# Kernel optimization log

Measured on AMD Instinct MI355X. Metric: run time of the kernel, lower is better.

## Reference

```python
import jax, jax.numpy as jnp
import numpy as np

DIM = 512
NUM_GROUPS = 32
EPS = 1e-6
INV_SQRT2 = 0.7071067811865476


def group_norm(x, gamma, beta):
    # x: [b, c, h, w]; GroupNorm with NUM_GROUPS groups, per-channel affine
    b, c, h, w = x.shape
    xg = x.reshape(b, NUM_GROUPS, c // NUM_GROUPS, h, w)
    mu = xg.mean(axis=(2, 3, 4), keepdims=True)
    var = xg.var(axis=(2, 3, 4), keepdims=True)
    xn = ((xg - mu) * jax.lax.rsqrt(var + EPS)).reshape(b, c, h, w)
    return xn * gamma[None, :, None, None] + beta[None, :, None, None]


def conv1x1(x, w, b):
    # 1x1 conv == per-pixel GEMM over channels. w: [out_c, in_c], b: [out_c]
    return jnp.einsum('oc,bchw->bohw', w, x) + b[None, :, None, None]


def setup_inputs() -> dict:
    key = jax.random.key(0)
    ks = jax.random.split(key, 6)
    b, c, h, w = 4, DIM, 64, 64
    q = jax.random.normal(ks[0], (b, c, h, w), dtype=jnp.float32)
    init = lambda k: jax.random.normal(k, (DIM, DIM), dtype=jnp.float32) * 0.02
    return {
        'q': q,
        'gamma': jnp.ones((DIM,), jnp.float32),
        'beta': jnp.zeros((DIM,), jnp.float32),
        'wq': init(ks[1]), 'bq': jnp.zeros((DIM,), jnp.float32),
        'wk': init(ks[2]), 'bk': jnp.zeros((DIM,), jnp.float32),
        'wv': init(ks[3]), 'bv': jnp.zeros((DIM,), jnp.float32),
        'wo': init(ks[4]), 'bo': jnp.zeros((DIM,), jnp.float32),
    }


def reference(q, gamma, beta, wq, bq, wk, bk, wv, bv, wo, bo):
    q_in = q
    x = group_norm(q, gamma, beta)  # self-attention path: v is None -> v = normed q
    qp = conv1x1(x, wq, bq)
    kp = conv1x1(x, wk, bk)
    vp = conv1x1(x, wv, bv)
    b, c, h, w = qp.shape
    qf = qp.reshape(b, c, h * w)
    kf = kp.reshape(b, c, h * w)
    vf = vp.reshape(b, c, h * w)
    # scores[b, i, j] = sum_c k[b,c,i] * q[b,c,j]; softmax over i (key axis, dim=-2)
    scores = jnp.einsum('bci,bcj->bij', kf, qf) * (c ** -0.5)
    attn = jax.nn.softmax(scores, axis=-2)
    out = jnp.einsum('bci,bij->bcj', vf, attn).reshape(b, c, h, w)
    out = conv1x1(out, wo, bo)
    return (out + q_in) * INV_SQRT2
```

## Files before the change

kernel.cpp:

```cpp
#include <hip/hip_runtime.h>

typedef __bf16 bf16;
typedef __bf16 bf16x4 __attribute__((ext_vector_type(4)));
typedef __bf16 bf16x8 __attribute__((ext_vector_type(8)));
typedef float floatx4 __attribute__((ext_vector_type(4)));
typedef float floatx16 __attribute__((ext_vector_type(16)));

#define SCALE_QK 0.044194173824159216f
#define INV_SQRT2F 0.7071067811865476f
#define TEN  8388608L
#define SBAT 2097152L

typedef const __attribute__((address_space(1))) void GV;
typedef __attribute__((address_space(3))) void SV;

__global__ __launch_bounds__(256) void detect_k(
    const unsigned* __restrict__ q, int* __restrict__ flag)
{
    __shared__ int cnt;
    if (threadIdx.x == 0) cnt = 0;
    __syncthreads();
    int c = 0;
    for (int i = threadIdx.x; i < 4096; i += 256) {
        unsigned e = (q[i] >> 7) & 0xFFu;
        c += (e >= 100u && e <= 140u) ? 1 : 0;
    }
    atomicAdd(&cnt, c);
    __syncthreads();
    if (threadIdx.x == 0) *flag = (cnt < 3000) ? 1 : 0;
}

__global__ __launch_bounds__(256) void convw_k(
    const void* w0, const void* w1, const void* w2, const void* w3,
    bf16* __restrict__ dst, const int* __restrict__ flag)
{
    const void* srcs[4] = {w0, w1, w2, w3};
    const void* s = srcs[blockIdx.y];
    bf16* d = dst + (size_t)blockIdx.y * 262144;
    const int i = (blockIdx.x * 256 + threadIdx.x) * 8;
    bf16x8 v;
    if (*flag) {
        const float* f = (const float*)s;
        #pragma unroll
        for (int r = 0; r < 8; ++r) v[r] = (bf16)f[i + r];
    } else {
        v = *(const bf16x8*)((const bf16*)s + i);
    }
    *(bf16x8*)(d + i) = v;
}

__global__ __launch_bounds__(256) void convp_k(
    const void* p0, const void* p1, const void* p2,
    const void* p3, const void* p4, const void* p5,
    float* __restrict__ dst, const int* __restrict__ flag)
{
    const void* srcs[6] = {p0, p1, p2, p3, p4, p5};
    const int f = *flag;
    for (int i = threadIdx.x; i < 3072; i += 256) {
        const void* s = srcs[i >> 9];
        const int off = i & 511;
        dst[i] = f ? ((const float*)s)[off] : (float)((const bf16*)s)[off];
    }
}

__global__ __launch_bounds__(256) void groupnorm_k(
    const void* __restrict__ qraw, const float* __restrict__ gamma,
    const float* __restrict__ beta, bf16* __restrict__ XN,
    const int* __restrict__ flag)
{
    const int tid = threadIdx.x;
    const int b = blockIdx.x >> 5, g = blockIdx.x & 31;
    const int f32 = *flag;
    const size_t base = ((size_t)b * 512 + (size_t)g * 16) * 4096;
    const float* sf = (const float*)qraw + base;
    const bf16*  sb = (const bf16*)qraw + base;

    float sum = 0.f, sq = 0.f;
    if (f32) {
        const floatx4* v4 = (const floatx4*)sf;
        for (int idx = tid; idx < 16384; idx += 256) {
            floatx4 v = v4[idx];
            #pragma unroll
            for (int r = 0; r < 4; ++r) { float f = v[r]; sum += f; sq += f * f; }
        }
    } else {
        const bf16x8* v8 = (const bf16x8*)sb;
        for (int idx = tid; idx < 8192; idx += 256) {
            bf16x8 v = v8[idx];
            #pragma unroll
            for (int r = 0; r < 8; ++r) { float f = (float)v[r]; sum += f; sq += f * f; }
        }
    }
    #pragma unroll
    for (int off = 32; off; off >>= 1) {
        sum += __shfl_down(sum, off);
        sq  += __shfl_down(sq, off);
    }
    __shared__ float sS[4], sQ[4];
    __shared__ float s_mean, s_rstd;
    const int wave = tid >> 6, lane = tid & 63;
    if (lane == 0) { sS[wave] = sum; sQ[wave] = sq; }
    __syncthreads();
    if (tid == 0) {
        float ts = sS[0] + sS[1] + sS[2] + sS[3];
        float tq = sQ[0] + sQ[1] + sQ[2] + sQ[3];
        float mean = ts * (1.0f / 65536.0f);
        float var  = tq * (1.0f / 65536.0f) - mean * mean;
        s_mean = mean;
        s_rstd = rsqrtf(fmaxf(var, 0.f) + 1e-6f);
    }
    __syncthreads();
    const float mean = s_mean, rstd = s_rstd;

    float ga[16], be[16];
    #pragma unroll
    for (int c = 0; c < 16; ++c) {
        ga[c] = gamma[g * 16 + c] * rstd;
        be[c] = beta[g * 16 + c] - mean * ga[c];
    }
    bf16* dst = XN + (size_t)b * SBAT + (size_t)g * 16;
    for (int p0 = 0; p0 < 4096; p0 += 256) {
        const int p = p0 + tid;
        bf16x8 o0, o1;
        #pragma unroll
        for (int c = 0; c < 8; ++c) {
            float v = f32 ? sf[(size_t)c * 4096 + p] : (float)sb[(size_t)c * 4096 + p];
            o0[c] = (bf16)(v * ga[c] + be[c]);
        }
        #pragma unroll
        for (int c = 0; c < 8; ++c) {
            float v = f32 ? sf[(size_t)(c + 8) * 4096 + p] : (float)sb[(size_t)(c + 8) * 4096 + p];
            o1[c] = (bf16)(v * ga[c + 8] + be[c + 8]);
        }
        bf16* dp = dst + (size_t)p * 512;
        *(bf16x8*)dp = o0;
        *(bf16x8*)(dp + 8) = o1;
    }
}

__global__ __launch_bounds__(512, 1) void fused_attn(
    const bf16* __restrict__ QKt,
    const bf16* __restrict__ V,
    bf16* __restrict__ AOt)
{
    __shared__ __align__(16) char smc[163840];

    const int tid = threadIdx.x;
    const int w = tid >> 6, lane = tid & 63;
    const int fr = lane & 15, quad = lane >> 4;
    const int l5 = lane >> 5, l31 = lane & 31;

    const int ll = blockIdx.x;
    const int xcd = ll & 7, rr = ll >> 3;
    const int b = xcd >> 1;
    const int j0 = ((xcd & 1) * 32 + rr) * 64;

    const bf16* Qb = QKt + (size_t)b * 4194304;
    const bf16* Kb = Qb + 512;
    const bf16* Vb = V + (size_t)b * SBAT;

    const int lcK = ((tid & 15) ^ ((tid >> 4) & 15)) << 3;
    const int rowK = tid >> 4;
    auto stageK = [&](int key0, int kd0, int buf) {
        char* d = smc + buf * 32768;
        const bf16* s0 = Kb + (size_t)(key0 + rowK) * 1024 + kd0 + lcK;
        #pragma unroll
        for (int rho = 0; rho < 4; ++rho)
            __builtin_amdgcn_global_load_lds((GV*)(s0 + (size_t)rho * 32 * 1024),
                (SV*)(d + rho * 8192 + tid * 16), 16, 0, 0);
    };
    const int lcV = ((tid & 3) ^ ((tid >> 3) & 3)) << 3;
    const int rowV = tid >> 2;
    auto stageV = [&](int i0, int buf) {
        char* d = smc + 65536 + buf * 32768;
        const bf16* s0 = Vb + (size_t)rowV * 4096 + i0 + lcV;
        #pragma unroll
        for (int rho = 0; rho < 4; ++rho)
            __builtin_amdgcn_global_load_lds((GV*)(s0 + (size_t)rho * 128 * 4096),
                (SV*)(d + rho * 8192 + tid * 16), 16, 0, 0);
    };
    auto stage_sub = [&](int cc, int s) {
        if (s < 3) {
            if (cc < 32) stageK(cc * 128, (s + 1) * 128, (s + 1) & 1);
            if (cc >= 1 && cc <= 32)
                stageV((cc - 1) * 128 + (s + 1) * 32, (s + 1) & 1);
        } else {
            if (cc < 31) stageK((cc + 1) * 128, 0, 0);
            if (cc < 32) stageV(cc * 128, 0);
        }
    };

    stageK(0, 0, 0);

    if (w < 4) {
        const int jb = w >> 1;
        const int kw = w & 1;
        bf16x8 qf[2][16];
        #pragma unroll
        for (int jj = 0; jj < 2; ++jj) {
            const bf16* qsrc = Qb +
                (size_t)(j0 + jb * 32 + jj * 16 + fr) * 1024 + quad * 8;
            #pragma unroll
            for (int s = 0; s < 16; ++s)
                qf[jj][s] = *(const bf16x8*)(qsrc + s * 32);
        }
        const int kbase = (kw * 64 + fr) * 256;
        const int pxor = fr << 4;
        const int prow0 = (jb * 32 + fr) * 256;
        const int pcol0 = kw * 128;
        float l_acc0 = 0.f, l_acc1 = 0.f;

        for (int cc = 0; cc <= 32; ++cc) {
            floatx4 acc_s[4][2] = {};
            #pragma unroll
            for (int s = 0; s < 4; ++s) {
                asm volatile("s_waitcnt vmcnt(0)" ::: "memory");
                __builtin_amdgcn_s_barrier();
                stage_sub(cc, s);
                if (cc < 32) {
                    const char* kbuf = smc + (s & 1) * 32768;
                    __builtin_amdgcn_s_setprio(1);
                    #pragma unroll
                    for (int ksl = 0; ksl < 4; ++ksl) {
                        bf16x8 kfr[4];
                        #pragma unroll
                        for (int kf = 0; kf < 4; ++kf)
                            kfr[kf] = *(const bf16x8*)(kbuf + kbase + kf * 4096 +
                                ((((ksl << 2) | quad) ^ fr) << 4));
                        #pragma unroll
                        for (int kf = 0; kf < 4; ++kf) {
                            acc_s[kf][0] = __builtin_amdgcn_mfma_f32_16x16x32_bf16(
                                kfr[kf], qf[0][s * 4 + ksl], acc_s[kf][0], 0, 0, 0);
                            acc_s[kf][1] = __builtin_amdgcn_mfma_f32_16x16x32_bf16(
                                kfr[kf], qf[1][s * 4 + ksl], acc_s[kf][1], 0, 0, 0);
                        }
                    }
                    __builtin_amdgcn_s_setprio(0);
                    if (s == 3) {
                        char* pb = smc + 131072 + (cc & 1) * 16384;
                        float rs0 = 0.f, rs1 = 0.f;
                        #pragma unroll
                        for (int kf = 0; kf < 4; ++kf) {
                            const int cb = (pcol0 + kf * 32 + quad * 8) ^ pxor;
                            bf16x4 pk0, pk1;
                            #pragma unroll
                            for (int r = 0; r < 4; ++r) {
                                float e0 = __expf(fminf(acc_s[kf][0][r] * SCALE_QK, 30.f));
                                float e1 = __expf(fminf(acc_s[kf][1][r] * SCALE_QK, 30.f));
                                rs0 += e0; rs1 += e1;
                                pk0[r] = (bf16)e0; pk1[r] = (bf16)e1;
                            }
                            *(bf16x4*)(pb + prow0 + cb) = pk0;
                            *(bf16x4*)(pb + prow0 + 4096 + cb) = pk1;
                        }
                        rs0 += __shfl_xor(rs0, 16);
                        rs0 += __shfl_xor(rs0, 32);
                        rs1 += __shfl_xor(rs1, 16);
                        rs1 += __shfl_xor(rs1, 32);
                        l_acc0 += rs0; l_acc1 += rs1;
                        asm volatile("s_waitcnt lgkmcnt(0)" ::: "memory");
                    }
                }
            }
        }
        __syncthreads();
        float* lp = (float*)smc;
        if (lane < 16) {
            lp[kw * 64 + jb * 32 + lane] = l_acc0;
            lp[kw * 64 + jb * 32 + 16 + lane] = l_acc1;
        }
        __syncthreads();
    } else {
        const int pw = w - 4;
        const int pxorR = (l31 & 15) << 4;
        floatx16 acc_o[2][4] = {};

        for (int cc = 0; cc <= 32; ++cc) {
            #pragma unroll
            for (int s = 0; s < 4; ++s) {
                asm volatile("s_waitcnt vmcnt(0)" ::: "memory");
                __builtin_amdgcn_s_barrier();
                stage_sub(cc, s);
                if (cc >= 1) {
                    const char* vb = smc + 65536 + (s & 1) * 32768;
                    const char* pb = smc + 131072 + ((cc - 1) & 1) * 16384;
                    __builtin_amdgcn_s_setprio(1);
                    #pragma unroll
                    for (int t = 0; t < 2; ++t) {
                        bf16x8 pa[2];
                        #pragma unroll
                        for (int jf = 0; jf < 2; ++jf)
                            pa[jf] = *(const bf16x8*)(pb + (jf * 32 + l31) * 256 +
                                (((s * 2 + t) * 32 + l5 * 16) ^ pxorR));
                        #pragma unroll
                        for (int nf = 0; nf < 4; ++nf) {
                            const int vc = pw * 128 + nf * 32 + l31;
                            bf16x8 vb8 = *(const bf16x8*)(vb + vc * 64 +
                                ((t * 32 + l5 * 16) ^ (((vc >> 1) & 3) << 4)));
                            acc_o[0][nf] = __builtin_amdgcn_mfma_f32_32x32x16_bf16(
                                pa[0], vb8, acc_o[0][nf], 0, 0, 0);
                            acc_o[1][nf] = __builtin_amdgcn_mfma_f32_32x32x16_bf16(
                                pa[1], vb8, acc_o[1][nf], 0, 0, 0);
                        }
                    }
                    __builtin_amdgcn_s_setprio(0);
                }
            }
        }
        __syncthreads();
        __syncthreads();
        const float* lp = (const float*)smc;

        bf16* out = AOt + (size_t)b * SBAT + (size_t)j0 * 512;
        #pragma unroll
        for (int jf = 0; jf < 2; ++jf) {
            #pragma unroll
            for (int reg = 0; reg < 16; ++reg) {
                const int j = jf * 32 + (reg & 3) + 8 * (reg >> 2) + 4 * l5;
                const float rl = 1.0f / fmaxf(lp[j] + lp[64 + j], 1e-30f);
                #pragma unroll
                for (int nf = 0; nf < 4; ++nf) {
                    const int d = pw * 128 + nf * 32 + l31;
                    out[(size_t)j * 512 + d] = (bf16)(acc_o[jf][nf][reg] * rl);
                }
            }
        }
    }
}

template <int EPI>
__global__ __launch_bounds__(256, 4) void gemm_xyt(
    const bf16* __restrict__ Xb, const bf16* __restrict__ Yb,
    void* __restrict__ Cv, int N, int K, int lda, int ldb,
    long sX, long sY, long sC,
    const float* __restrict__ bias,
    const void* __restrict__ res, long sR,
    const int* __restrict__ flag)
{
    __shared__ __align__(16) bf16 smem[17408];

    const int tid  = threadIdx.x;
    const int wave = tid >> 6;
    const int lane = tid & 63;
    const int z = blockIdx.z;

    int bx = blockIdx.x, by = blockIdx.y;
    {
        const int gx = gridDim.x, gy = gridDim.y;
        const int o = by * gx + bx;
        const int xcd = o & 7, idx = o >> 3;
        if (gx == 8) {
            bx = xcd;
            by = idx;
        } else if (gx == 32 && gy == 4) {
            bx = (xcd & 1) * 16 + (idx & 15);
            by = xcd >> 1;
        }
    }

    const bf16* X = Xb + (long)z * sX;
    const bf16* Y = Yb + (long)z * sY;
    bf16*  Cb = (bf16*)Cv  + (long)z * sC;
    float* Cf = (float*)Cv + (long)z * sC;
    const int f32o = (EPI == 4) ? *flag : 0;

    const int m0 = by * 128, n0 = bx * 128;
    const int wm = (wave >> 1) * 64, wn = (wave & 1) * 64;
    const int fr = lane & 15, quad = lane >> 4;

    const int srow = tid >> 2;
    const int scol = (tid & 3) * 8;
    const bf16* pX = X + (size_t)(m0 + srow) * lda + scol;
    const bf16* pY = Y + (size_t)(n0 + srow) * ldb + scol;
    const size_t oX = (size_t)64 * lda, oY = (size_t)64 * ldb;
    char* const sb0 = (char*)smem;
    const int ldst = tid * 16;

    auto stage = [&](int k, int pb) {
        char* d = sb0 + pb * 16384;
        const bf16* x = pX + k * 32;
        const bf16* y = pY + k * 32;
        __builtin_amdgcn_global_load_lds((GV*)x,        (SV*)(d + ldst),         16, 0, 0);
        __builtin_amdgcn_global_load_lds((GV*)(x + oX), (SV*)(d + 4096 + ldst),  16, 0, 0);
        __builtin_amdgcn_global_load_lds((GV*)y,        (SV*)(d + 8192 + ldst),  16, 0, 0);
        __builtin_amdgcn_global_load_lds((GV*)(y + oY), (SV*)(d + 12288 + ldst), 16, 0, 0);
    };

    floatx4 acc[4][4] = {};
    const int NK = K >> 5;

    stage(0, 0);
    __syncthreads();

    for (int k = 0; k < NK; ++k) {
        const int p = k & 1;
        if (k + 1 < NK) stage(k + 1, 1 - p);
        const bf16* bA = smem + p * 8192;
        const bf16* bB = bA + 4096;
        bf16x8 af[4], bfr[4];
        #pragma unroll
        for (int i = 0; i < 4; ++i) {
            af[i]  = *(const bf16x8*)&bA[(wm + i * 16 + fr) * 32 + quad * 8];
            bfr[i] = *(const bf16x8*)&bB[(wn + i * 16 + fr) * 32 + quad * 8];
        }
        #pragma unroll
        for (int i = 0; i < 4; ++i)
            #pragma unroll
            for (int j = 0; j < 4; ++j)
                acc[i][j] = __builtin_amdgcn_mfma_f32_16x16x32_bf16(
                    af[i], bfr[j], acc[i][j], 0, 0, 0);
        __syncthreads();
    }

    #pragma unroll
    for (int i = 0; i < 4; ++i) {
        const int mg = m0 + wm + i * 16 + quad * 4;
        float bmr[4];
        if (EPI == 1 || EPI == 4) {
            #pragma unroll
            for (int r = 0; r < 4; ++r) bmr[r] = bias[mg + r];
        }
        #pragma unroll
        for (int j = 0; j < 4; ++j) {
            const int ng = n0 + wn + j * 16 + fr;
            #pragma unroll
            for (int r = 0; r < 4; ++r) {
                float v = acc[i][j][r];
                if (EPI == 0) v += bias[ng];
                if (EPI == 1) v += bmr[r];
                if (EPI == 4) v += bmr[r];
                acc[i][j][r] = v;
            }
        }
    }

    if (EPI != 4) {
        bf16* ct = smem;
        #pragma unroll
        for (int i = 0; i < 4; ++i)
            #pragma unroll
            for (int j = 0; j < 4; ++j)
                #pragma unroll
                for (int r = 0; r < 4; ++r)
                    ct[(wm + i * 16 + quad * 4 + r) * 132 + wn + j * 16 + fr] =
                        (bf16)acc[i][j][r];
        __syncthreads();
        #pragma unroll
        for (int w = 0; w < 8; ++w) {
            const int idx = w * 2048 + tid * 8;
            const int row = idx >> 7, col = idx & 127;
            bf16x8 v = *(const bf16x8*)&ct[row * 132 + col];
            *(bf16x8*)&Cb[(size_t)(m0 + row) * N + n0 + col] = v;
        }
    } else if (f32o) {
        float* ct = (float*)smem;
        const float* rres = (const float*)res + (size_t)z * sR;
        #pragma unroll
        for (int h = 0; h < 2; ++h) {
            if ((wave >> 1) == h) {
                #pragma unroll
                for (int i = 0; i < 4; ++i)
                    #pragma unroll
                    for (int j = 0; j < 4; ++j)
                        #pragma unroll
                        for (int r = 0; r < 4; ++r)
                            ct[(i * 16 + quad * 4 + r) * 132 + wn + j * 16 + fr] =
                                acc[i][j][r];
            }
            __syncthreads();
            #pragma unroll
            for (int w = 0; w < 8; ++w) {
                const int idx = (w * 256 + tid) * 4;
                const int row = idx >> 7, col = idx & 127;
                const size_t o = (size_t)(m0 + h * 64 + row) * N + n0 + col;
                floatx4 v = *(const floatx4*)&ct[row * 132 + col];
                floatx4 rv = *(const floatx4*)&rres[o];
                #pragma unroll
                for (int e = 0; e < 4; ++e) v[e] = (v[e] + rv[e]) * INV_SQRT2F;
                *(floatx4*)&Cf[o] = v;
            }
            __syncthreads();
        }
    } else {
        const bf16* resb = (const bf16*)res + (size_t)z * sR;
        #pragma unroll
        for (int i = 0; i < 4; ++i) {
            const int mg = m0 + wm + i * 16 + quad * 4;
            #pragma unroll
            for (int j = 0; j < 4; ++j) {
                const int ng = n0 + wn + j * 16 + fr;
                #pragma unroll
                for (int r = 0; r < 4; ++r) {
                    const size_t o = (size_t)(mg + r) * N + ng;
                    Cb[o] = (bf16)((acc[i][j][r] + (float)resb[o]) * INV_SQRT2F);
                }
            }
        }
    }
}

extern "C" void kernel_launch(void* const* d_in, const int* in_sizes, int n_in,
                              void* d_out, int out_size, void* d_ws, size_t ws_size,
                              hipStream_t stream)
{
    const void* q     = d_in[0];
    const void* gamma = d_in[1];
    const void* beta  = d_in[2];
    const void* wq    = d_in[3];
    const void* bq    = d_in[4];
    const void* wk    = d_in[5];
    const void* bk    = d_in[6];
    const void* wv    = d_in[7];
    const void* bv    = d_in[8];
    const void* wo    = d_in[9];
    const void* bo    = d_in[10];

    char* w = (char*)d_ws;
    int*   flag = (int*)w;   w += 16;
    float* Pf   = (float*)w; w += 6 * 512 * 4;
    bf16*  Wc   = (bf16*)w;  w += 4 * 262144 * 2;
    bf16*  XN   = (bf16*)w;  w += TEN * 2;
    bf16*  QKt  = (bf16*)w;  w += (size_t)4 * 4096 * 1024 * 2;
    bf16*  V    = (bf16*)w;  w += TEN * 2;
    bf16*  AOt  = XN;

    detect_k<<<dim3(1), 256, 0, stream>>>((const unsigned*)q, flag);
    convw_k<<<dim3(128, 4), 256, 0, stream>>>(wq, wk, wv, wo, Wc, flag);
    convp_k<<<dim3(1), 256, 0, stream>>>(gamma, beta, bq, bk, bv, bo, Pf, flag);

    groupnorm_k<<<dim3(128), 256, 0, stream>>>(q, Pf, Pf + 512, XN, flag);

    gemm_xyt<0><<<dim3(8, 32, 4), 256, 0, stream>>>(XN, Wc, QKt,
        1024, 512, 512, 512, SBAT, 0, (long)4096 * 1024, Pf + 1024,
        nullptr, 0, flag);
    gemm_xyt<1><<<dim3(32, 4, 4), 256, 0, stream>>>(Wc + 2 * 262144, XN, V,
        4096, 512, 512, 512, 0, SBAT, SBAT, Pf + 2048,
        nullptr, 0, flag);

    fused_attn<<<dim3(256), 512, 0, stream>>>(QKt, V, AOt);

    gemm_xyt<4><<<dim3(32, 4, 4), 256, 0, stream>>>(Wc + 3 * 262144, AOt, d_out,
        4096, 512, 512, 512, 0, SBAT, SBAT, Pf + 2560,
        q, SBAT, flag);
}
```

Before: 444.2 us.

## Deepen K/V staging pipeline to four smaller buffers with partial vmcnt waits

Splits each 128-key chunk into eight smaller sub-stages, each staging 64 K dims and 16 V keys into one of four 16KB ring buffers. Loads are issued three stages ahead, and the wait uses vmcnt(8) instead of a full drain. The aim is to keep more global-to-LDS loads in flight and stop waves stalling on vmcnt(0) at every barrier. In exchange there are twice as many barriers per chunk, less MFMA work between them, and some redundant clamped loads at the edges of the pipeline.

```diff
diff --git a/kernel.cpp b/kernel.cpp
--- a/kernel.cpp
+++ b/kernel.cpp
@@ -159,38 +159,27 @@
     const bf16* Kb = Qb + 512;
     const bf16* Vb = V + (size_t)b * SBAT;
 
-    const int lcK = ((tid & 15) ^ ((tid >> 4) & 15)) << 3;
-    const int rowK = tid >> 4;
-    auto stageK = [&](int key0, int kd0, int buf) {
-        char* d = smc + buf * 32768;
-        const bf16* s0 = Kb + (size_t)(key0 + rowK) * 1024 + kd0 + lcK;
-        #pragma unroll
-        for (int rho = 0; rho < 4; ++rho)
-            __builtin_amdgcn_global_load_lds((GV*)(s0 + (size_t)rho * 32 * 1024),
-                (SV*)(d + rho * 8192 + tid * 16), 16, 0, 0);
+    const int krow0 = tid >> 3;
+    const int klog  = ((tid & 7) ^ ((tid >> 3) & 7)) << 3;
+    const int vrow0 = tid >> 1;
+    const int vlog  = ((tid & 1) ^ ((tid >> 3) & 1)) << 3;
+
+    auto stage_for = [&](int kcc, int ks, int vcc, int vs, int buf) {
+        {
+            char* d = smc + buf * 16384 + tid * 16;
+            const bf16* s0 = Kb + (size_t)(kcc * 128 + krow0) * 1024 + ks * 64 + klog;
+            __builtin_amdgcn_global_load_lds((GV*)s0, (SV*)d, 16, 0, 0);
+            __builtin_amdgcn_global_load_lds((GV*)(s0 + (size_t)64 * 1024),
+                                             (SV*)(d + 8192), 16, 0, 0);
+        }
+        {
+            char* d = smc + 65536 + buf * 16384 + tid * 16;
+            const bf16* s0 = Vb + (size_t)vrow0 * 4096 + vcc * 128 + vs * 16 + vlog;
+            __builtin_amdgcn_global_load_lds((GV*)s0, (SV*)d, 16, 0, 0);
+            __builtin_amdgcn_global_load_lds((GV*)(s0 + (size_t)256 * 4096),
+                                             (SV*)(d + 8192), 16, 0, 0);
+        }
     };
-    const int lcV = ((tid & 3) ^ ((tid >> 3) & 3)) << 3;
-    const int rowV = tid >> 2;
-    auto stageV = [&](int i0, int buf) {
-        char* d = smc + 65536 + buf * 32768;
-        const bf16* s0 = Vb + (size_t)rowV * 4096 + i0 + lcV;
-        #pragma unroll
-        for (int rho = 0; rho < 4; ++rho)
-            __builtin_amdgcn_global_load_lds((GV*)(s0 + (size_t)rho * 128 * 4096),
-                (SV*)(d + rho * 8192 + tid * 16), 16, 0, 0);
-    };
-    auto stage_sub = [&](int cc, int s) {
-        if (s < 3) {
-            if (cc < 32) stageK(cc * 128, (s + 1) * 128, (s + 1) & 1);
-            if (cc >= 1 && cc <= 32)
-                stageV((cc - 1) * 128 + (s + 1) * 32, (s + 1) & 1);
-        } else {
-            if (cc < 31) stageK((cc + 1) * 128, 0, 0);
-            if (cc < 32) stageV(cc * 128, 0);
-        }
-    };
-
-    stageK(0, 0, 0);
 
     if (w < 4) {
         const int jb = w >> 1;
@@ -204,39 +193,49 @@
             for (int s = 0; s < 16; ++s)
                 qf[jj][s] = *(const bf16x8*)(qsrc + s * 32);
         }
-        const int kbase = (kw * 64 + fr) * 256;
         const int pxor = fr << 4;
         const int prow0 = (jb * 32 + fr) * 256;
         const int pcol0 = kw * 128;
         float l_acc0 = 0.f, l_acc1 = 0.f;
 
+        stage_for(0, 0, 0, 0, 0);
+        stage_for(0, 1, 0, 1, 1);
+        stage_for(0, 2, 0, 2, 2);
+
         for (int cc = 0; cc <= 32; ++cc) {
             floatx4 acc_s[4][2] = {};
             #pragma unroll
-            for (int s = 0; s < 4; ++s) {
-                asm volatile("s_waitcnt vmcnt(0)" ::: "memory");
+            for (int s = 0; s < 8; ++s) {
+                asm volatile("s_waitcnt vmcnt(8)" ::: "memory");
                 __builtin_amdgcn_s_barrier();
-                stage_sub(cc, s);
+                {
+                    const int cy = (s + 3) >> 3, ts = (s + 3) & 7, bu = (s + 3) & 3;
+                    const int kcc = (cc + cy > 31) ? 31 : cc + cy;
+                    int vcc = cc + cy - 1;
+                    vcc = (vcc < 0) ? 0 : ((vcc > 31) ? 31 : vcc);
+                    stage_for(kcc, ts, vcc, ts, bu);
+                }
                 if (cc < 32) {
-                    const char* kbuf = smc + (s & 1) * 32768;
+                    const char* kbuf = smc + (s & 3) * 16384;
                     __builtin_amdgcn_s_setprio(1);
                     #pragma unroll
-                    for (int ksl = 0; ksl < 4; ++ksl) {
+                    for (int ksl = 0; ksl < 2; ++ksl) {
                         bf16x8 kfr[4];
                         #pragma unroll
                         for (int kf = 0; kf < 4; ++kf)
-                            kfr[kf] = *(const bf16x8*)(kbuf + kbase + kf * 4096 +
-                                ((((ksl << 2) | quad) ^ fr) << 4));
+                            kfr[kf] = *(const bf16x8*)(kbuf +
+                                (kw * 64 + kf * 16 + fr) * 128 +
+                                (((ksl * 4 + quad) ^ (fr & 7)) << 4));
                         #pragma unroll
                         for (int kf = 0; kf < 4; ++kf) {
                             acc_s[kf][0] = __builtin_amdgcn_mfma_f32_16x16x32_bf16(
-                                kfr[kf], qf[0][s * 4 + ksl], acc_s[kf][0], 0, 0, 0);
+                                kfr[kf], qf[0][s * 2 + ksl], acc_s[kf][0], 0, 0, 0);
                             acc_s[kf][1] = __builtin_amdgcn_mfma_f32_16x16x32_bf16(
-                                kfr[kf], qf[1][s * 4 + ksl], acc_s[kf][1], 0, 0, 0);
+                                kfr[kf], qf[1][s * 2 + ksl], acc_s[kf][1], 0, 0, 0);
                         }
                     }
                     __builtin_amdgcn_s_setprio(0);
-                    if (s == 3) {
+                    if (s == 7) {
                         char* pb = smc + 131072 + (cc & 1) * 16384;
                         float rs0 = 0.f, rs1 = 0.f;
                         #pragma unroll
@@ -272,36 +271,42 @@
         __syncthreads();
     } else {
         const int pw = w - 4;
-        const int pxorR = (l31 & 15) << 4;
         floatx16 acc_o[2][4] = {};
 
+        stage_for(0, 0, 0, 0, 0);
+        stage_for(0, 1, 0, 1, 1);
+        stage_for(0, 2, 0, 2, 2);
+
         for (int cc = 0; cc <= 32; ++cc) {
             #pragma unroll
-            for (int s = 0; s < 4; ++s) {
-                asm volatile("s_waitcnt vmcnt(0)" ::: "memory");
+            for (int s = 0; s < 8; ++s) {
+                asm volatile("s_waitcnt vmcnt(8)" ::: "memory");
                 __builtin_amdgcn_s_barrier();
-                stage_sub(cc, s);
+                {
+                    const int cy = (s + 3) >> 3, ts = (s + 3) & 7, bu = (s + 3) & 3;
+                    const int kcc = (cc + cy > 31) ? 31 : cc + cy;
+                    int vcc = cc + cy - 1;
+                    vcc = (vcc < 0) ? 0 : ((vcc > 31) ? 31 : vcc);
+                    stage_for(kcc, ts, vcc, ts, bu);
+                }
                 if (cc >= 1) {
-                    const char* vb = smc + 65536 + (s & 1) * 32768;
+                    const char* vb = smc + 65536 + (s & 3) * 16384;
                     const char* pb = smc + 131072 + ((cc - 1) & 1) * 16384;
                     __builtin_amdgcn_s_setprio(1);
+                    bf16x8 pa[2];
                     #pragma unroll
-                    for (int t = 0; t < 2; ++t) {
-                        bf16x8 pa[2];
-                        #pragma unroll
-                        for (int jf = 0; jf < 2; ++jf)
-                            pa[jf] = *(const bf16x8*)(pb + (jf * 32 + l31) * 256 +
-                                (((s * 2 + t) * 32 + l5 * 16) ^ pxorR));
-                        #pragma unroll
-                        for (int nf = 0; nf < 4; ++nf) {
-                            const int vc = pw * 128 + nf * 32 + l31;
-                            bf16x8 vb8 = *(const bf16x8*)(vb + vc * 64 +
-                                ((t * 32 + l5 * 16) ^ (((vc >> 1) & 3) << 4)));
-                            acc_o[0][nf] = __builtin_amdgcn_mfma_f32_32x32x16_bf16(
-                                pa[0], vb8, acc_o[0][nf], 0, 0, 0);
-                            acc_o[1][nf] = __builtin_amdgcn_mfma_f32_32x32x16_bf16(
-                                pa[1], vb8, acc_o[1][nf], 0, 0, 0);
-                        }
+                    for (int jf = 0; jf < 2; ++jf)
+                        pa[jf] = *(const bf16x8*)(pb + (jf * 32 + l31) * 256 +
+                            (((s * 2 + l5) ^ (l31 & 15)) << 4));
+                    #pragma unroll
+                    for (int nf = 0; nf < 4; ++nf) {
+                        const int vc = pw * 128 + nf * 32 + l31;
+                        bf16x8 vb8 = *(const bf16x8*)(vb + vc * 32 +
+                            ((l5 ^ ((vc >> 2) & 1)) << 4));
+                        acc_o[0][nf] = __builtin_amdgcn_mfma_f32_32x32x16_bf16(
+                            pa[0], vb8, acc_o[0][nf], 0, 0, 0);
+                        acc_o[1][nf] = __builtin_amdgcn_mfma_f32_32x32x16_bf16(
+                            pa[1], vb8, acc_o[1][nf], 0, 0, 0);
                     }
                     __builtin_amdgcn_s_setprio(0);
                 }
```

After: 513.1 us. 15.5% more time.

## Merge prep kernels and stage groupnorm half-slab in LDS to avoid re-reading input

Applied to the files above, without the earlier changes.

Folds the dtype-detection, weight-conversion and parameter-conversion kernels into one launch, with each block recomputing the detection flag itself. This removes two launches and their serial dependency. Groupnorm now runs on 256 blocks, each handling half of a group's pixels. During the statistics pass each block caches its half of the input in LDS, so the normalize pass reads LDS instead of global memory. Each block still reads the whole group to compute the statistics, which doubles the stats-pass traffic, and the roughly 131KB of LDS per block limits occupancy to one block per CU.

```diff
diff --git a/kernel.cpp b/kernel.cpp
--- a/kernel.cpp
+++ b/kernel.cpp
@@ -14,8 +14,12 @@
 typedef const __attribute__((address_space(1))) void GV;
 typedef __attribute__((address_space(3))) void SV;
 
-__global__ __launch_bounds__(256) void detect_k(
-    const unsigned* __restrict__ q, int* __restrict__ flag)
+__global__ __launch_bounds__(256) void prep_k(
+    const unsigned* __restrict__ q,
+    const void* w0, const void* w1, const void* w2, const void* w3,
+    const void* p0, const void* p1, const void* p2,
+    const void* p3, const void* p4, const void* p5,
+    bf16* __restrict__ Wc, float* __restrict__ Pf, int* __restrict__ flagp)
 {
     __shared__ int cnt;
     if (threadIdx.x == 0) cnt = 0;
@@ -27,39 +31,32 @@
     }
     atomicAdd(&cnt, c);
     __syncthreads();
-    if (threadIdx.x == 0) *flag = (cnt < 3000) ? 1 : 0;
-}
-
-__global__ __launch_bounds__(256) void convw_k(
-    const void* w0, const void* w1, const void* w2, const void* w3,
-    bf16* __restrict__ dst, const int* __restrict__ flag)
-{
-    const void* srcs[4] = {w0, w1, w2, w3};
-    const void* s = srcs[blockIdx.y];
-    bf16* d = dst + (size_t)blockIdx.y * 262144;
-    const int i = (blockIdx.x * 256 + threadIdx.x) * 8;
-    bf16x8 v;
-    if (*flag) {
-        const float* f = (const float*)s;
-        #pragma unroll
-        for (int r = 0; r < 8; ++r) v[r] = (bf16)f[i + r];
+    const int flag = (cnt < 3000) ? 1 : 0;
+
+    const int blk = blockIdx.x;
+    if (blk < 512) {
+        const void* srcs[4] = {w0, w1, w2, w3};
+        const int wy = blk >> 7, bx = blk & 127;
+        const void* s = srcs[wy];
+        bf16* d = Wc + (size_t)wy * 262144;
+        const int i = (bx * 256 + threadIdx.x) * 8;
+        bf16x8 v;
+        if (flag) {
+            const float* f = (const float*)s;
+            #pragma unroll
+            for (int r = 0; r < 8; ++r) v[r] = (bf16)f[i + r];
+        } else {
+            v = *(const bf16x8*)((const bf16*)s + i);
+        }
+        *(bf16x8*)(d + i) = v;
     } else {
-        v = *(const bf16x8*)((const bf16*)s + i);
-    }
-    *(bf16x8*)(d + i) = v;
-}
-
-__global__ __launch_bounds__(256) void convp_k(
-    const void* p0, const void* p1, const void* p2,
-    const void* p3, const void* p4, const void* p5,
-    float* __restrict__ dst, const int* __restrict__ flag)
-{
-    const void* srcs[6] = {p0, p1, p2, p3, p4, p5};
-    const int f = *flag;
-    for (int i = threadIdx.x; i < 3072; i += 256) {
-        const void* s = srcs[i >> 9];
-        const int off = i & 511;
-        dst[i] = f ? ((const float*)s)[off] : (float)((const bf16*)s)[off];
+        if (threadIdx.x == 0) *flagp = flag;
+        const void* srcs[6] = {p0, p1, p2, p3, p4, p5};
+        for (int i = threadIdx.x; i < 3072; i += 256) {
+            const void* s = srcs[i >> 9];
+            const int off = i & 511;
+            Pf[i] = flag ? ((const float*)s)[off] : (float)((const bf16*)s)[off];
+        }
     }
 }
 
@@ -68,8 +65,9 @@
     const float* __restrict__ beta, bf16* __restrict__ XN,
     const int* __restrict__ flag)
 {
+    __shared__ float Xs[16 * 2052];
     const int tid = threadIdx.x;
-    const int b = blockIdx.x >> 5, g = blockIdx.x & 31;
+    const int b = blockIdx.x >> 6, g = (blockIdx.x >> 1) & 31, h = blockIdx.x & 1;
     const int f32 = *flag;
     const size_t base = ((size_t)b * 512 + (size_t)g * 16) * 4096;
     const float* sf = (const float*)qraw + base;
@@ -80,15 +78,28 @@
         const floatx4* v4 = (const floatx4*)sf;
         for (int idx = tid; idx < 16384; idx += 256) {
             floatx4 v = v4[idx];
+            const int c = idx >> 10, px4 = idx & 1023;
             #pragma unroll
             for (int r = 0; r < 4; ++r) { float f = v[r]; sum += f; sq += f * f; }
+            if ((px4 >> 9) == h) {
+                float* d = &Xs[c * 2052 + px4 * 4 - h * 2048];
+                #pragma unroll
+                for (int r = 0; r < 4; ++r) d[r] = v[r];
+            }
         }
     } else {
         const bf16x8* v8 = (const bf16x8*)sb;
         for (int idx = tid; idx < 8192; idx += 256) {
             bf16x8 v = v8[idx];
-            #pragma unroll
-            for (int r = 0; r < 8; ++r) { float f = (float)v[r]; sum += f; sq += f * f; }
+            const int c = idx >> 9, px8 = idx & 511;
+            float fv[8];
+            #pragma unroll
+            for (int r = 0; r < 8; ++r) { fv[r] = (float)v[r]; sum += fv[r]; sq += fv[r] * fv[r]; }
+            if ((px8 >> 8) == h) {
+                float* d = &Xs[c * 2052 + px8 * 8 - h * 2048];
+                #pragma unroll
+                for (int r = 0; r < 8; ++r) d[r] = fv[r];
+            }
         }
     }
     #pragma unroll
@@ -119,19 +130,16 @@
         be[c] = beta[g * 16 + c] - mean * ga[c];
     }
     bf16* dst = XN + (size_t)b * SBAT + (size_t)g * 16;
-    for (int p0 = 0; p0 < 4096; p0 += 256) {
-        const int p = p0 + tid;
+    for (int p0 = 0; p0 < 2048; p0 += 256) {
+        const int pl = p0 + tid;
+        const int p = h * 2048 + pl;
         bf16x8 o0, o1;
         #pragma unroll
-        for (int c = 0; c < 8; ++c) {
-            float v = f32 ? sf[(size_t)c * 4096 + p] : (float)sb[(size_t)c * 4096 + p];
-            o0[c] = (bf16)(v * ga[c] + be[c]);
-        }
-        #pragma unroll
-        for (int c = 0; c < 8; ++c) {
-            float v = f32 ? sf[(size_t)(c + 8) * 4096 + p] : (float)sb[(size_t)(c + 8) * 4096 + p];
-            o1[c] = (bf16)(v * ga[c + 8] + be[c + 8]);
-        }
+        for (int c = 0; c < 8; ++c)
+            o0[c] = (bf16)(Xs[c * 2052 + pl] * ga[c] + be[c]);
+        #pragma unroll
+        for (int c = 0; c < 8; ++c)
+            o1[c] = (bf16)(Xs[(c + 8) * 2052 + pl] * ga[c + 8] + be[c + 8]);
         bf16* dp = dst + (size_t)p * 512;
         *(bf16x8*)dp = o0;
         *(bf16x8*)(dp + 8) = o1;
@@ -524,11 +532,10 @@
     bf16*  V    = (bf16*)w;  w += TEN * 2;
     bf16*  AOt  = XN;
 
-    detect_k<<<dim3(1), 256, 0, stream>>>((const unsigned*)q, flag);
-    convw_k<<<dim3(128, 4), 256, 0, stream>>>(wq, wk, wv, wo, Wc, flag);
-    convp_k<<<dim3(1), 256, 0, stream>>>(gamma, beta, bq, bk, bv, bo, Pf, flag);
-
-    groupnorm_k<<<dim3(128), 256, 0, stream>>>(q, Pf, Pf + 512, XN, flag);
+    prep_k<<<dim3(513), 256, 0, stream>>>((const unsigned*)q,
+        wq, wk, wv, wo, gamma, beta, bq, bk, bv, bo, Wc, Pf, flag);
+
+    groupnorm_k<<<dim3(256), 256, 0, stream>>>(q, Pf, Pf + 512, XN, flag);
 
     gemm_xyt<0><<<dim3(8, 32, 4), 256, 0, stream>>>(XN, Wc, QKt,
         1024, 512, 512, 512, SBAT, 0, (long)4096 * 1024, Pf + 1024,
```

New measurement: 432.9 us. 1.03x faster.
